# Optimization experiments

Hardware: AMD Instinct MI355X
Metric: run time of the kernel (lower is better)

## Reference

```python
import jax, jax.numpy as jnp
import numpy as np

B, V, F_IN, F_HID = 1000000, 9, 5, 3


def setup_inputs() -> dict:
    key = jax.random.key(0)
    k1, k2, k3, k4, k5 = jax.random.split(key, 5)
    A = jax.random.uniform(k1, (B, V, V), dtype=jnp.float32)
    h0 = jax.random.uniform(k2, (B, V, F_IN), dtype=jnp.float32)
    # learned params (match torch init scales loosely)
    W = jax.random.uniform(k3, (F_IN, F_HID), dtype=jnp.float32) * 0.01
    fc_w = jax.random.normal(k4, (F_HID, 1), dtype=jnp.float32) * 0.1
    fc_b = jnp.zeros((1,), dtype=jnp.float32)
    return {"A": A, "h0": h0, "W": W, "fc_w": fc_w, "fc_b": fc_b}


def reference(A, h0, W, fc_w, fc_b):
    # GCN layer, batched (replaces per-sample Python loop)
    V_ = A.shape[-1]
    AI = A + jnp.eye(V_, dtype=A.dtype)                 # A + I, [B,V,V]
    deg = jnp.sum(AI, axis=-2)                          # torch.sum(AI, 0): column sums, [B,V]
    dinv = 1.0 / jnp.sqrt(deg)                          # diag of D^{-1/2}
    DAD = dinv[..., :, None] * AI * dinv[..., None, :]  # D^-1/2 (A+I) D^-1/2
    HW = jnp.einsum('bvf,fh->bvh', h0, W)               # H W
    h1 = jax.nn.relu(jnp.einsum('bvu,buh->bvh', DAD, HW))
    # graph pooling: sum over nodes
    h2 = jnp.sum(h1, axis=1)                            # [B, F_HID]
    return h2 @ fc_w + fc_b                             # [B, 1]
```

## Files before the change

### kernel.cpp

```cpp
#include <hip/hip_runtime.h>

#define NV 9
#define FIN 5
#define FHID 3
#define A_ELEMS (NV*NV)
#define H_ELEMS (NV*FIN)
#define TPB 256

__device__ __forceinline__ float4 ld16(const float* p) {
    float4 v;
    __builtin_memcpy(&v, p, 16);
    return v;
}

__global__ __launch_bounds__(TPB, 2) void gcn_direct_kernel(
    const float* __restrict__ A, const float* __restrict__ h0,
    const float* __restrict__ W, const float* __restrict__ fc_w,
    const float* __restrict__ fc_b, float* __restrict__ out, int Btot)
{
    const int i = blockIdx.x * TPB + threadIdx.x;
    if (i >= Btot) return;

    const float* __restrict__ Ai = A  + (long long)i * A_ELEMS;
    const float* __restrict__ Hi = h0 + (long long)i * H_ELEMS;

    float a[A_ELEMS];
#pragma unroll
    for (int j = 0; j < 20; j++) {
        float4 v = ld16(Ai + 4 * j);
        a[4*j+0] = v.x; a[4*j+1] = v.y; a[4*j+2] = v.z; a[4*j+3] = v.w;
    }
    a[80] = Ai[80];

    float Wr[FIN * FHID];
#pragma unroll
    for (int k = 0; k < FIN * FHID; k++) Wr[k] = W[k];
    const float fw0 = fc_w[0], fw1 = fc_w[1], fw2 = fc_w[2];
    const float fb = fc_b[0];

    float G[NV * FHID];
#pragma unroll
    for (int u = 0; u < NV; u++) {
        float4 v = ld16(Hi + u * FIN);
        const float h4 = Hi[u * FIN + 4];
        const float hr[FIN] = {v.x, v.y, v.z, v.w, h4};
#pragma unroll
        for (int h = 0; h < FHID; h++) {
            float acc = 0.0f;
#pragma unroll
            for (int f = 0; f < FIN; f++) acc += hr[f] * Wr[f * FHID + h];
            G[u * FHID + h] = acc;
        }
    }

    float deg[NV];
#pragma unroll
    for (int j = 0; j < NV; j++) deg[j] = 1.0f;
#pragma unroll
    for (int r = 0; r < NV; r++) {
#pragma unroll
        for (int j = 0; j < NV; j++) deg[j] += a[r * NV + j];
    }
    float dinv[NV];
#pragma unroll
    for (int j = 0; j < NV; j++) dinv[j] = 1.0f / sqrtf(deg[j]);

#pragma unroll
    for (int u = 0; u < NV; u++) {
#pragma unroll
        for (int h = 0; h < FHID; h++) G[u * FHID + h] *= dinv[u];
    }

    float h2_0 = 0.0f, h2_1 = 0.0f, h2_2 = 0.0f;
#pragma unroll
    for (int v = 0; v < NV; v++) {
        float a0 = 0.0f, a1 = 0.0f, a2 = 0.0f;
#pragma unroll
        for (int u = 0; u < NV; u++) {
            const float aiv = a[v * NV + u] + ((u == v) ? 1.0f : 0.0f);
            a0 += aiv * G[u * FHID + 0];
            a1 += aiv * G[u * FHID + 1];
            a2 += aiv * G[u * FHID + 2];
        }
        const float dv = dinv[v];
        h2_0 += fmaxf(a0 * dv, 0.0f);
        h2_1 += fmaxf(a1 * dv, 0.0f);
        h2_2 += fmaxf(a2 * dv, 0.0f);
    }

    out[i] = h2_0 * fw0 + h2_1 * fw1 + h2_2 * fw2 + fb;
}

extern "C" void kernel_launch(void* const* d_in, const int* in_sizes, int n_in,
                              void* d_out, int out_size, void* d_ws, size_t ws_size,
                              hipStream_t stream) {
    const float* A    = (const float*)d_in[0];
    const float* h0   = (const float*)d_in[1];
    const float* W    = (const float*)d_in[2];
    const float* fc_w = (const float*)d_in[3];
    const float* fc_b = (const float*)d_in[4];
    float* out = (float*)d_out;

    const int Btot = in_sizes[0] / A_ELEMS;
    const int grid = (Btot + TPB - 1) / TPB;

    gcn_direct_kernel<<<grid, TPB, 0, stream>>>(A, h0, W, fc_w, fc_b, out, Btot);
}
```

Before: 546.3 us.

## Stage A through LDS with coalesced global_load_lds in 64-thread blocks

Each block now handles 64 samples: the block's contiguous A chunk is copied cooperatively and fully coalesced into shared memory using global_load_lds, and each thread then reads its own 9x9 matrix from LDS. Before, every thread issued strided per-sample 16-byte loads. h0 is loaded per thread as a contiguous 45-float vector, and the HW product is fused with the dinv scaling. The cost is LDS traffic with a stride-81 access pattern that may cause bank conflicts, plus small 64-thread blocks that each need a full barrier.

```diff
diff --git a/kernel.cpp b/kernel.cpp
--- a/kernel.cpp
+++ b/kernel.cpp
@@ -3,9 +3,16 @@
 #define NV 9
 #define FIN 5
 #define FHID 3
+#define SPB 64
 #define A_ELEMS (NV*NV)
 #define H_ELEMS (NV*FIN)
-#define TPB 256
+#define A_CHUNK (SPB*A_ELEMS)
+
+__device__ __forceinline__ void load_lds16(const float* g, float* l) {
+    __builtin_amdgcn_global_load_lds(
+        (const __attribute__((address_space(1))) unsigned int*)g,
+        (__attribute__((address_space(3))) unsigned int*)l, 16, 0, 0);
+}
 
 __device__ __forceinline__ float4 ld16(const float* p) {
     float4 v;
@@ -13,24 +20,41 @@
     return v;
 }
 
-__global__ __launch_bounds__(TPB, 2) void gcn_direct_kernel(
+__global__ __launch_bounds__(64) void gcn_hybrid_kernel(
     const float* __restrict__ A, const float* __restrict__ h0,
     const float* __restrict__ W, const float* __restrict__ fc_w,
     const float* __restrict__ fc_b, float* __restrict__ out, int Btot)
 {
-    const int i = blockIdx.x * TPB + threadIdx.x;
-    if (i >= Btot) return;
+    __shared__ float sA[A_CHUNK];
 
-    const float* __restrict__ Ai = A  + (long long)i * A_ELEMS;
-    const float* __restrict__ Hi = h0 + (long long)i * H_ELEMS;
+    const int tid = threadIdx.x;
+    const long long base = (long long)blockIdx.x * SPB;
+    const int cnt = (Btot - (int)base < SPB) ? (Btot - (int)base) : SPB;
+    const float* gA = A + base * A_ELEMS;
 
-    float a[A_ELEMS];
+    if (cnt == SPB) {
 #pragma unroll
-    for (int j = 0; j < 20; j++) {
-        float4 v = ld16(Ai + 4 * j);
-        a[4*j+0] = v.x; a[4*j+1] = v.y; a[4*j+2] = v.z; a[4*j+3] = v.w;
+        for (int j = 0; j < 20; j++)
+            load_lds16(gA + j * 256 + tid * 4, sA + j * 256 + tid * 4);
+        if (tid < 16)
+            load_lds16(gA + 20 * 256 + tid * 4, sA + 20 * 256 + tid * 4);
+    } else {
+        const int nA = cnt * A_ELEMS;
+        for (int i = tid; i < nA; i += SPB) sA[i] = gA[i];
     }
-    a[80] = Ai[80];
+
+    const bool active = tid < cnt;
+    float h[H_ELEMS];
+    if (active) {
+        const float* Hi = h0 + (base + tid) * H_ELEMS;
+#pragma unroll
+        for (int j = 0; j < 11; j++) {
+            float4 v = ld16(Hi + 4 * j);
+            h[4*j+0] = v.x; h[4*j+1] = v.y;
+            h[4*j+2] = v.z; h[4*j+3] = v.w;
+        }
+        h[44] = Hi[44];
+    }
 
     float Wr[FIN * FHID];
 #pragma unroll
@@ -38,20 +62,16 @@
     const float fw0 = fc_w[0], fw1 = fc_w[1], fw2 = fc_w[2];
     const float fb = fc_b[0];
 
-    float G[NV * FHID];
+    asm volatile("s_waitcnt vmcnt(0) lgkmcnt(0)" ::: "memory");
+    __syncthreads();
+
+    if (!active) return;
+
+    const float* Ai = sA + tid * A_ELEMS;
+
+    float a[A_ELEMS];
 #pragma unroll
-    for (int u = 0; u < NV; u++) {
-        float4 v = ld16(Hi + u * FIN);
-        const float h4 = Hi[u * FIN + 4];
-        const float hr[FIN] = {v.x, v.y, v.z, v.w, h4};
-#pragma unroll
-        for (int h = 0; h < FHID; h++) {
-            float acc = 0.0f;
-#pragma unroll
-            for (int f = 0; f < FIN; f++) acc += hr[f] * Wr[f * FHID + h];
-            G[u * FHID + h] = acc;
-        }
-    }
+    for (int i = 0; i < A_ELEMS; i++) a[i] = Ai[i];
 
     float deg[NV];
 #pragma unroll
@@ -65,10 +85,16 @@
 #pragma unroll
     for (int j = 0; j < NV; j++) dinv[j] = 1.0f / sqrtf(deg[j]);
 
+    float G[NV * FHID];
 #pragma unroll
     for (int u = 0; u < NV; u++) {
 #pragma unroll
-        for (int h = 0; h < FHID; h++) G[u * FHID + h] *= dinv[u];
+        for (int hh = 0; hh < FHID; hh++) {
+            float acc = 0.0f;
+#pragma unroll
+            for (int f = 0; f < FIN; f++) acc += h[u * FIN + f] * Wr[f * FHID + hh];
+            G[u * FHID + hh] = dinv[u] * acc;
+        }
     }
 
     float h2_0 = 0.0f, h2_1 = 0.0f, h2_2 = 0.0f;
@@ -88,7 +114,7 @@
         h2_2 += fmaxf(a2 * dv, 0.0f);
     }
 
-    out[i] = h2_0 * fw0 + h2_1 * fw1 + h2_2 * fw2 + fb;
+    out[base + tid] = h2_0 * fw0 + h2_1 * fw1 + h2_2 * fw2 + fb;
 }
 
 extern "C" void kernel_launch(void* const* d_in, const int* in_sizes, int n_in,
@@ -102,7 +128,7 @@
     float* out = (float*)d_out;
 
     const int Btot = in_sizes[0] / A_ELEMS;
-    const int grid = (Btot + TPB - 1) / TPB;
+    const int grid = (Btot + SPB - 1) / SPB;
 
-    gcn_direct_kernel<<<grid, TPB, 0, stream>>>(A, h0, W, fc_w, fc_b, out, Btot);
+    gcn_hybrid_kernel<<<grid, SPB, 0, stream>>>(A, h0, W, fc_w, fc_b, out, Btot);
 }
```

New measurement: 524.5 us. 4.0% less time.
